# Kernel tuning notes

Measured on AMD Instinct MI355X. Metric: run time of the kernel, lower is better.

The kernel has to match this reference:

```python
import jax, jax.numpy as jnp
import numpy as np

N = 50000
NUM_USERS = 20000
E = 800000
IN_DIM = 256
OUT_DIM = 256
H = 8
DK = OUT_DIM // H


def setup_inputs() -> dict:
    key = jax.random.key(0)
    ks = jax.random.split(key, 16)
    inp = {
        "x": jax.random.normal(ks[0], (N, IN_DIM), dtype=jnp.float32),
        "row": jax.random.randint(ks[1], (E,), 0, N, dtype=jnp.int32),
        "col": jax.random.randint(ks[2], (E,), 0, N, dtype=jnp.int32),
        "relation_emb": jax.random.normal(ks[3], (OUT_DIM,), dtype=jnp.float32),
        "user_text_embs": jax.random.normal(ks[4], (NUM_USERS, IN_DIM), dtype=jnp.float32),
        "item_text_embs": jax.random.normal(ks[5], (N - NUM_USERS, IN_DIM), dtype=jnp.float32),
        "Wq": jax.random.normal(ks[6], (OUT_DIM, IN_DIM), dtype=jnp.float32) * 0.02,
        "bq": jnp.zeros((OUT_DIM,), dtype=jnp.float32),
        "Wk": jax.random.normal(ks[7], (OUT_DIM, IN_DIM), dtype=jnp.float32) * 0.02,
        "bk": jnp.zeros((OUT_DIM,), dtype=jnp.float32),
        "Wv": jax.random.normal(ks[8], (OUT_DIM, IN_DIM), dtype=jnp.float32) * 0.02,
        "bv": jnp.zeros((OUT_DIM,), dtype=jnp.float32),
        "Wo": jax.random.normal(ks[9], (OUT_DIM, OUT_DIM), dtype=jnp.float32) * 0.02,
        "bo": jnp.zeros((OUT_DIM,), dtype=jnp.float32),
    }
    return inp


def reference(x, row, col, relation_emb, user_text_embs, item_text_embs,
              Wq, bq, Wk, bk, Wv, bv, Wo, bo):
    # text_emb: users first, then items (matches torch zeros_like + slice assign)
    text_emb = jnp.concatenate([user_text_embs, item_text_embs], axis=0)  # [N, in_dim]

    Q = (text_emb @ Wq.T + bq).reshape(N, H, DK)
    K = (text_emb @ Wk.T + bk).reshape(N, H, DK)
    V = (x @ Wv.T + bv).reshape(N, H, DK)

    Q_ = Q[col]  # [E, H, DK]
    K_ = K[row]
    V_ = V[row]
    rel = relation_emb.reshape(1, H, DK)

    scores = jnp.sum(Q_ * (K_ + rel), axis=-1) / np.sqrt(DK).astype(np.float32)  # [E, H]

    # segment softmax over destination node (col)
    m = jax.ops.segment_max(scores, col, num_segments=N)          # [N, H]
    e = jnp.exp(scores - m[col])                                   # [E, H]
    denom = jax.ops.segment_sum(e, col, num_segments=N)           # [N, H]
    attn = e / denom[col]                                          # [E, H]

    out = jax.ops.segment_sum(attn[:, :, None] * V_, col, num_segments=N)  # [N, H, DK]
    out = out.reshape(N, OUT_DIM)
    return out @ Wo.T + bo
```

## Files before the change

### kernel.cpp

```cpp
#include <hip/hip_runtime.h>
#include <hip/hip_bf16.h>

#define N_NODES   50000
#define N_USERS   20000
#define N_EDGES   800000
#define DIM       256
#define NHEAD     8
#define DKH       32
#define NBLK_SCAN ((N_NODES + 255) / 256)
#define NGRP      (N_NODES / 16)
#define NGRP_PAD  3128
#define SLOTS_NODE (NGRP * 8 * 64)
#define NBLK_CAST (SLOTS_NODE / 256)
#define NBLK_HIST ((N_EDGES + 255) / 256)
#define NBLK_G64  (NGRP_PAD / 4)
#define KVROW     768

typedef __attribute__((ext_vector_type(8))) short bf16x8;
typedef __attribute__((ext_vector_type(4))) float f32x4;
typedef __attribute__((ext_vector_type(4))) unsigned short u16x4;
typedef __attribute__((ext_vector_type(8))) unsigned short u16x8;

__device__ inline unsigned short f2bf(float f) {
    union { __hip_bfloat16 b; unsigned short u; } cv;
    cv.b = __float2bfloat16(f);
    return cv.u;
}
__device__ inline float bf2f(unsigned short u) {
    return __uint_as_float(((unsigned int)u) << 16);
}
__device__ inline unsigned char f2fp8(float f) {
    unsigned int p = __builtin_amdgcn_cvt_pk_fp8_f32(f, f, 0, false);
    return (unsigned char)(p & 0xff);
}


__global__ void prep_kernel(const float* __restrict__ Wq, const float* __restrict__ Wk,
                            const float* __restrict__ Wv, const float* __restrict__ Wo,
                            unsigned short* __restrict__ Wb2,
                            const float* __restrict__ x,
                            const float* __restrict__ user, const float* __restrict__ item,
                            unsigned short* __restrict__ xb2, unsigned short* __restrict__ tb2,
                            const int* __restrict__ col, int* __restrict__ cnt)
{
    int b = blockIdx.x;
    if (b < 128) {
        int gid = b * 256 + threadIdx.x;
        const float* srcs[4] = { Wq, Wk, Wv, Wo };
        int m = gid >> 13, slot = gid & 8191;
        int lane = slot & 63, ks = (slot >> 6) & 7, g = slot >> 9;
        int c = g * 16 + (lane & 15);
        int d = ks * 32 + (lane >> 4) * 8;
        const float* s = srcs[m] + (size_t)c * DIM + d;
        float4 f0 = *(const float4*)s, f1 = *(const float4*)(s + 4);
        u16x8 o = { f2bf(f0.x), f2bf(f0.y), f2bf(f0.z), f2bf(f0.w),
                    f2bf(f1.x), f2bf(f1.y), f2bf(f1.z), f2bf(f1.w) };
        *(u16x8*)(Wb2 + (size_t)m * 65536 + (size_t)slot * 8) = o;
    } else if (b < 128 + NBLK_CAST) {
        int slot = (b - 128) * 256 + threadIdx.x;
        int lane = slot & 63, ks = (slot >> 6) & 7, g = slot >> 9;
        int r = g * 16 + (lane & 15);
        int d = ks * 32 + (lane >> 4) * 8;

        const float* sx = x + (size_t)r * DIM + d;
        float4 f0 = *(const float4*)sx, f1 = *(const float4*)(sx + 4);
        u16x8 xo = { f2bf(f0.x), f2bf(f0.y), f2bf(f0.z), f2bf(f0.w),
                     f2bf(f1.x), f2bf(f1.y), f2bf(f1.z), f2bf(f1.w) };
        *(u16x8*)(xb2 + (size_t)slot * 8) = xo;

        const float* st = (r < N_USERS) ? user + (size_t)r * DIM + d
                                        : item + (size_t)(r - N_USERS) * DIM + d;
        float4 t0 = *(const float4*)st, t1 = *(const float4*)(st + 4);
        u16x8 to = { f2bf(t0.x), f2bf(t0.y), f2bf(t0.z), f2bf(t0.w),
                     f2bf(t1.x), f2bf(t1.y), f2bf(t1.z), f2bf(t1.w) };
        *(u16x8*)(tb2 + (size_t)slot * 8) = to;
    } else {
        int e = (b - 128 - NBLK_CAST) * 256 + threadIdx.x;
        if (e < N_EDGES) atomicAdd(&cnt[col[e]], 1);
    }
}

__device__ __forceinline__ void mfma_core64(const unsigned short* __restrict__ A2,
                                            const unsigned short* __restrict__ W2,
                                            int row0, f32x4 acc[2][8],
                                            int lane, int wid)
{
    const int gA = (row0 >> 4) + (wid >> 1) * 2;
    const int gB = (wid & 1) * 8;
    #pragma unroll
    for (int ks = 0; ks < 8; ++ks) {
        bf16x8 a[2], b[8];
        #pragma unroll
        for (int i = 0; i < 2; ++i)
            a[i] = *(const bf16x8*)(A2 + (size_t)((gA + i) * 8 + ks) * 512 + lane * 8);
        #pragma unroll
        for (int j = 0; j < 8; ++j)
            b[j] = *(const bf16x8*)(W2 + (size_t)((gB + j) * 8 + ks) * 512 + lane * 8);
        #pragma unroll
        for (int i = 0; i < 2; ++i)
            #pragma unroll
            for (int j = 0; j < 8; ++j)
                acc[i][j] = __builtin_amdgcn_mfma_f32_16x16x32_bf16(a[i], b[j], acc[i][j], 0, 0, 0);
    }
}

template<int MODE>
__device__ __forceinline__ void epilogue64(f32x4 acc[2][8], const float* bias, void* Cv,
                                           int row0, int M, int lane, int wid)
{
    const int wm = wid >> 1, wn = wid & 1;
    const int lr = lane & 15, lk = lane >> 4;
    float* Cf = (float*)Cv;
    unsigned short* Cb = (unsigned short*)Cv;
    unsigned char* C8 = (unsigned char*)Cv;
    #pragma unroll
    for (int i = 0; i < 2; ++i) {
        #pragma unroll
        for (int r = 0; r < 4; ++r) {
            int grow = row0 + wm * 32 + i * 16 + lk * 4 + r;
            if (grow >= M) continue;
            #pragma unroll
            for (int j = 0; j < 8; ++j) {
                int gcol = wn * 128 + j * 16 + lr;
                float val = acc[i][j][r] + bias[gcol];
                if constexpr (MODE == 0) {
                    Cf[(size_t)grow * 256 + gcol] = val;
                } else if constexpr (MODE == 1) {
                    Cb[(size_t)grow * 256 + gcol] = f2bf(val);
                } else if constexpr (MODE == 2) {
                    C8[(size_t)grow * KVROW + gcol] = f2fp8(val);
                } else {
                    *(unsigned short*)(C8 + (size_t)grow * KVROW + 256 + gcol * 2) = f2bf(val);
                }
            }
        }
    }
}

__global__ __launch_bounds__(256) void gemm_qkv_reg(
    const unsigned short* __restrict__ tb2, const unsigned short* __restrict__ xb2,
    const unsigned short* __restrict__ Wb2,
    const float* __restrict__ bq, const float* __restrict__ bk, const float* __restrict__ bv,
    unsigned short* __restrict__ Qb, unsigned char* __restrict__ KVb, int M)
{
    const int tid = threadIdx.x;
    const int lane = tid & 63, wid = tid >> 6;
    const int row0 = blockIdx.x * 64;
    const int mat  = blockIdx.y;

    const unsigned short* A2 = (mat == 2) ? xb2 : tb2;
    const unsigned short* W2 = Wb2 + (size_t)mat * 65536;

    f32x4 acc[2][8];
    #pragma unroll
    for (int i = 0; i < 2; ++i)
        #pragma unroll
        for (int j = 0; j < 8; ++j) acc[i][j] = (f32x4){0.f, 0.f, 0.f, 0.f};

    mfma_core64(A2, W2, row0, acc, lane, wid);

    if (mat == 0)      epilogue64<1>(acc, bq, Qb,  row0, M, lane, wid);
    else if (mat == 1) epilogue64<2>(acc, bk, KVb, row0, M, lane, wid);
    else               epilogue64<3>(acc, bv, KVb, row0, M, lane, wid);
}

__global__ __launch_bounds__(256) void gemm_o_reg(
    const unsigned short* __restrict__ A2,
    const unsigned short* __restrict__ Wb2, const float* __restrict__ bo,
    float* __restrict__ C, int M)
{
    const int tid = threadIdx.x;
    const int lane = tid & 63, wid = tid >> 6;
    const int row0 = blockIdx.x * 64;

    f32x4 acc[2][8];
    #pragma unroll
    for (int i = 0; i < 2; ++i)
        #pragma unroll
        for (int j = 0; j < 8; ++j) acc[i][j] = (f32x4){0.f, 0.f, 0.f, 0.f};

    mfma_core64(A2, Wb2 + 3 * 65536, row0, acc, lane, wid);
    epilogue64<0>(acc, bo, C, row0, M, lane, wid);
}

__global__ __launch_bounds__(256) void scan_blk_kernel(const int* __restrict__ cnt,
                                                       int* __restrict__ offs_tmp,
                                                       int* __restrict__ bsum) {
    __shared__ int s[256];
    int b = blockIdx.x, t = threadIdx.x;
    int i = b * 256 + t;
    int v = (i < N_NODES) ? cnt[i] : 0;
    s[t] = v;
    __syncthreads();
    #pragma unroll
    for (int d = 1; d < 256; d <<= 1) {
        int u = (t >= d) ? s[t - d] : 0;
        __syncthreads();
        s[t] += u;
        __syncthreads();
    }
    if (i < N_NODES) offs_tmp[i] = s[t] - v;
    if (t == 255) bsum[b] = s[255];
}

__global__ __launch_bounds__(256) void scan_top_kernel(int* __restrict__ bsum) {
    __shared__ int s[256];
    int t = threadIdx.x;
    int v = (t < NBLK_SCAN) ? bsum[t] : 0;
    s[t] = v;
    __syncthreads();
    #pragma unroll
    for (int d = 1; d < 256; d <<= 1) {
        int u = (t >= d) ? s[t - d] : 0;
        __syncthreads();
        s[t] += u;
        __syncthreads();
    }
    if (t < NBLK_SCAN) bsum[t] = s[t] - v;
}

__global__ __launch_bounds__(256) void scan_add_kernel(const int* __restrict__ offs_tmp,
                                                       const int* __restrict__ bsum,
                                                       int* __restrict__ offs,
                                                       int* __restrict__ cursor) {
    int i = blockIdx.x * 256 + threadIdx.x;
    if (i == 0) offs[N_NODES] = N_EDGES;
    if (i >= N_NODES) return;
    int o = offs_tmp[i] + bsum[blockIdx.x];
    offs[i] = o;
    cursor[i] = o;
}

__global__ void scatter_kernel(const int* __restrict__ row, const int* __restrict__ col,
                               int* __restrict__ cursor, int* __restrict__ esrc) {
    int e = blockIdx.x * blockDim.x + threadIdx.x;
    if (e >= N_EDGES) return;
    int c = col[e];
    int p = atomicAdd(&cursor[c], 1);
    esrc[p] = row[e];
}

__global__ __launch_bounds__(256) void node_fused_kernel(
    const unsigned short* __restrict__ Qb, const unsigned char* __restrict__ KVb,
    const float* __restrict__ rel,
    const int* __restrict__ offs, const int* __restrict__ esrc,
    unsigned short* __restrict__ outagg2)
{
    const float SC = 0.17677669529663687f;
    int wid = (blockIdx.x * blockDim.x + threadIdx.x) >> 6;
    int lane = threadIdx.x & 63;
    if (wid >= N_NODES) return;
    int beg = offs[wid], end = offs[wid + 1];
    int d0 = lane * 4;
    const unsigned char* kbase = KVb + lane * 4;
    const unsigned char* vbase = KVb + 256 + lane * 8;

    u16x4 qb4 = *(const u16x4*)(Qb + (size_t)wid * DIM + d0);
    float qx = bf2f(qb4[0]), qy = bf2f(qb4[1]), qz = bf2f(qb4[2]), qw = bf2f(qb4[3]);
    float4 rl = *(const float4*)(rel + d0);

    float p0 = qx * rl.x + qy * rl.y + qz * rl.z + qw * rl.w;
    p0 += __shfl_xor(p0, 1);
    p0 += __shfl_xor(p0, 2);
    p0 += __shfl_xor(p0, 4);

    float den = 0.f;
    float4 acc = make_float4(0.f, 0.f, 0.f, 0.f);

    for (int base = beg; base < end; base += 64) {
        int n = end - base; if (n > 64) n = 64;
        int idx = base + lane; if (idx >= end) idx = end - 1;
        int my = esrc[idx];
        int j = 0;
        for (; j + 8 <= n; j += 8) {
            unsigned int kw[8]; u16x4 vv[8];
            #pragma unroll
            for (int u = 0; u < 8; ++u) {
                int r = __shfl(my, j + u);
                size_t ro = (size_t)r * KVROW;
                kw[u] = *(const unsigned int*)(kbase + ro);
                vv[u] = *(const u16x4*)(vbase + ro);
            }
            float s[8];
            #pragma unroll
            for (int u = 0; u < 8; ++u)
                s[u] = qx * __builtin_amdgcn_cvt_f32_fp8(kw[u], 0)
                     + qy * __builtin_amdgcn_cvt_f32_fp8(kw[u], 1)
                     + qz * __builtin_amdgcn_cvt_f32_fp8(kw[u], 2)
                     + qw * __builtin_amdgcn_cvt_f32_fp8(kw[u], 3);
            #pragma unroll
            for (int u = 0; u < 8; ++u) {
                s[u] += __shfl_xor(s[u], 1);
                s[u] += __shfl_xor(s[u], 2);
                s[u] += __shfl_xor(s[u], 4);
            }
            #pragma unroll
            for (int u = 0; u < 8; ++u) {
                float w = __expf((s[u] + p0) * SC);
                den += w;
                acc.x += w * bf2f(vv[u][0]); acc.y += w * bf2f(vv[u][1]);
                acc.z += w * bf2f(vv[u][2]); acc.w += w * bf2f(vv[u][3]);
            }
        }
        for (; j + 4 <= n; j += 4) {
            unsigned int kw[4]; u16x4 vv[4];
            #pragma unroll
            for (int u = 0; u < 4; ++u) {
                int r = __shfl(my, j + u);
                size_t ro = (size_t)r * KVROW;
                kw[u] = *(const unsigned int*)(kbase + ro);
                vv[u] = *(const u16x4*)(vbase + ro);
            }
            float s[4];
            #pragma unroll
            for (int u = 0; u < 4; ++u)
                s[u] = qx * __builtin_amdgcn_cvt_f32_fp8(kw[u], 0)
                     + qy * __builtin_amdgcn_cvt_f32_fp8(kw[u], 1)
                     + qz * __builtin_amdgcn_cvt_f32_fp8(kw[u], 2)
                     + qw * __builtin_amdgcn_cvt_f32_fp8(kw[u], 3);
            #pragma unroll
            for (int u = 0; u < 4; ++u) {
                s[u] += __shfl_xor(s[u], 1);
                s[u] += __shfl_xor(s[u], 2);
                s[u] += __shfl_xor(s[u], 4);
            }
            #pragma unroll
            for (int u = 0; u < 4; ++u) {
                float w = __expf((s[u] + p0) * SC);
                den += w;
                acc.x += w * bf2f(vv[u][0]); acc.y += w * bf2f(vv[u][1]);
                acc.z += w * bf2f(vv[u][2]); acc.w += w * bf2f(vv[u][3]);
            }
        }
        for (; j < n; ++j) {
            int r = __shfl(my, j);
            size_t ro = (size_t)r * KVROW;
            unsigned int kw = *(const unsigned int*)(kbase + ro);
            u16x4 vv = *(const u16x4*)(vbase + ro);
            float s0 = qx * __builtin_amdgcn_cvt_f32_fp8(kw, 0)
                     + qy * __builtin_amdgcn_cvt_f32_fp8(kw, 1)
                     + qz * __builtin_amdgcn_cvt_f32_fp8(kw, 2)
                     + qw * __builtin_amdgcn_cvt_f32_fp8(kw, 3);
            s0 += __shfl_xor(s0, 1);
            s0 += __shfl_xor(s0, 2);
            s0 += __shfl_xor(s0, 4);
            float w0 = __expf((s0 + p0) * SC);
            den += w0;
            acc.x += w0 * bf2f(vv[0]); acc.y += w0 * bf2f(vv[1]);
            acc.z += w0 * bf2f(vv[2]); acc.w += w0 * bf2f(vv[3]);
        }
    }
    float rden = (end > beg) ? 1.f / den : 0.f;
    u16x4 o = { f2bf(acc.x * rden), f2bf(acc.y * rden),
                f2bf(acc.z * rden), f2bf(acc.w * rden) };
    int ks = lane >> 3, lk = (lane >> 1) & 3, e4 = (lane & 1) * 4;
    size_t toff = ((size_t)(wid >> 4) * 8 + ks) * 512 + (lk * 16 + (wid & 15)) * 8 + e4;
    *(u16x4*)(outagg2 + toff) = o;
}

extern "C" void kernel_launch(void* const* d_in, const int* in_sizes, int n_in,
                              void* d_out, int out_size, void* d_ws, size_t ws_size,
                              hipStream_t stream) {
    const float* x    = (const float*)d_in[0];
    const int*   row  = (const int*)d_in[1];
    const int*   col  = (const int*)d_in[2];
    const float* rel  = (const float*)d_in[3];
    const float* user = (const float*)d_in[4];
    const float* item = (const float*)d_in[5];
    const float* Wq   = (const float*)d_in[6];
    const float* bq   = (const float*)d_in[7];
    const float* Wk   = (const float*)d_in[8];
    const float* bk   = (const float*)d_in[9];
    const float* Wv   = (const float*)d_in[10];
    const float* bv   = (const float*)d_in[11];
    const float* Wo   = (const float*)d_in[12];
    const float* bo   = (const float*)d_in[13];

    char* ws = (char*)d_ws;
    size_t off = 0;
    auto alloc = [&](size_t bytes) -> void* {
        void* p = ws + off;
        off = (off + bytes + 255) & ~(size_t)255;
        return p;
    };
    const size_t tiled_sz = (size_t)NGRP_PAD * 4096 * 2;
    unsigned short* Qb      = (unsigned short*)alloc((size_t)N_NODES * DIM * 2);
    unsigned char*  KVb     = (unsigned char*)alloc((size_t)N_NODES * KVROW);
    unsigned short* xb2     = (unsigned short*)alloc(tiled_sz);
    unsigned short* tb2     = (unsigned short*)alloc(tiled_sz);
    unsigned short* outagg2 = (unsigned short*)alloc(tiled_sz);
    unsigned short* Wb2     = (unsigned short*)alloc((size_t)4 * 65536 * 2);
    int*   cnt      = (int*)alloc((size_t)N_NODES * 4);
    int*   offs     = (int*)alloc((size_t)(N_NODES + 1) * 4);
    int*   offs_tmp = (int*)alloc((size_t)N_NODES * 4);
    int*   bsum     = (int*)alloc((size_t)NBLK_SCAN * 4);
    int*   esrc     = (int*)alloc((size_t)N_EDGES * 4);

    hipMemsetAsync(cnt, 0, (size_t)N_NODES * 4, stream);

    prep_kernel<<<128 + NBLK_CAST + NBLK_HIST, 256, 0, stream>>>(
        Wq, Wk, Wv, Wo, Wb2, x, user, item, xb2, tb2, col, cnt);
    scan_blk_kernel<<<NBLK_SCAN, 256, 0, stream>>>(cnt, offs_tmp, bsum);
    scan_top_kernel<<<1, 256, 0, stream>>>(bsum);
    scan_add_kernel<<<NBLK_SCAN, 256, 0, stream>>>(offs_tmp, bsum, offs, cnt);
    scatter_kernel<<<NBLK_HIST, 256, 0, stream>>>(row, col, cnt, esrc);

    gemm_qkv_reg<<<dim3(NBLK_G64, 3), 256, 0, stream>>>(tb2, xb2, Wb2, bq, bk, bv, Qb, KVb, N_NODES);

    node_fused_kernel<<<(N_NODES * 64 + 255) / 256, 256, 0, stream>>>(
        Qb, KVb, rel, offs, esrc, outagg2);

    gemm_o_reg<<<NBLK_G64, 256, 0, stream>>>(outagg2, Wb2, bo, (float*)d_out, N_NODES);
}
```

Baseline: 279.7 us.

## Record edge ranks in histogram and fuse CSR scatter into QKV GEMM launch

The histogram atomics now store each edge's rank within its destination bucket. This lets the scatter compute positions as offs+rank without a second round of atomics. The scatter work is then merged into the QKV GEMM launch as extra leading blocks, which removes one kernel launch and lets the scatter overlap with the GEMM. The cost is an extra 3.2MB rank buffer that is written and then read, plus a mixed grid that may interfere with GEMM block scheduling.

```diff
diff --git a/kernel.cpp b/kernel.cpp
--- a/kernel.cpp
+++ b/kernel.cpp
@@ -41,7 +41,8 @@
                             const float* __restrict__ x,
                             const float* __restrict__ user, const float* __restrict__ item,
                             unsigned short* __restrict__ xb2, unsigned short* __restrict__ tb2,
-                            const int* __restrict__ col, int* __restrict__ cnt)
+                            const int* __restrict__ col, int* __restrict__ cnt,
+                            int* __restrict__ erank)
 {
     int b = blockIdx.x;
     if (b < 128) {
@@ -76,7 +77,7 @@
         *(u16x8*)(tb2 + (size_t)slot * 8) = to;
     } else {
         int e = (b - 128 - NBLK_CAST) * 256 + threadIdx.x;
-        if (e < N_EDGES) atomicAdd(&cnt[col[e]], 1);
+        if (e < N_EDGES) erank[e] = atomicAdd(&cnt[col[e]], 1);
     }
 }
 
@@ -137,16 +138,29 @@
     }
 }
 
-__global__ __launch_bounds__(256) void gemm_qkv_reg(
+__global__ __launch_bounds__(256) void gemm_qkv_scatter(
     const unsigned short* __restrict__ tb2, const unsigned short* __restrict__ xb2,
     const unsigned short* __restrict__ Wb2,
     const float* __restrict__ bq, const float* __restrict__ bk, const float* __restrict__ bv,
-    unsigned short* __restrict__ Qb, unsigned char* __restrict__ KVb, int M)
-{
+    unsigned short* __restrict__ Qb, unsigned char* __restrict__ KVb, int M,
+    const int* __restrict__ row, const int* __restrict__ col,
+    const int* __restrict__ erank, const int* __restrict__ offs,
+    int* __restrict__ esrc)
+{
+    const int b = blockIdx.x;
+    if (b < NBLK_HIST) {
+        int e = b * 256 + threadIdx.x;
+        if (e < N_EDGES) {
+            int c = col[e];
+            esrc[offs[c] + erank[e]] = row[e];
+        }
+        return;
+    }
+    const int gb = b - NBLK_HIST;
+    const int mat = gb / NBLK_G64;
+    const int row0 = (gb % NBLK_G64) * 64;
     const int tid = threadIdx.x;
     const int lane = tid & 63, wid = tid >> 6;
-    const int row0 = blockIdx.x * 64;
-    const int mat  = blockIdx.y;
 
     const unsigned short* A2 = (mat == 2) ? xb2 : tb2;
     const unsigned short* W2 = Wb2 + (size_t)mat * 65536;
@@ -221,23 +235,11 @@
 
 __global__ __launch_bounds__(256) void scan_add_kernel(const int* __restrict__ offs_tmp,
                                                        const int* __restrict__ bsum,
-                                                       int* __restrict__ offs,
-                                                       int* __restrict__ cursor) {
+                                                       int* __restrict__ offs) {
     int i = blockIdx.x * 256 + threadIdx.x;
     if (i == 0) offs[N_NODES] = N_EDGES;
     if (i >= N_NODES) return;
-    int o = offs_tmp[i] + bsum[blockIdx.x];
-    offs[i] = o;
-    cursor[i] = o;
-}
-
-__global__ void scatter_kernel(const int* __restrict__ row, const int* __restrict__ col,
-                               int* __restrict__ cursor, int* __restrict__ esrc) {
-    int e = blockIdx.x * blockDim.x + threadIdx.x;
-    if (e >= N_EDGES) return;
-    int c = col[e];
-    int p = atomicAdd(&cursor[c], 1);
-    esrc[p] = row[e];
+    offs[i] = offs_tmp[i] + bsum[blockIdx.x];
 }
 
 __global__ __launch_bounds__(256) void node_fused_kernel(
@@ -395,17 +397,19 @@
     int*   offs_tmp = (int*)alloc((size_t)N_NODES * 4);
     int*   bsum     = (int*)alloc((size_t)NBLK_SCAN * 4);
     int*   esrc     = (int*)alloc((size_t)N_EDGES * 4);
+    int*   erank    = (int*)alloc((size_t)N_EDGES * 4);
 
     hipMemsetAsync(cnt, 0, (size_t)N_NODES * 4, stream);
 
     prep_kernel<<<128 + NBLK_CAST + NBLK_HIST, 256, 0, stream>>>(
-        Wq, Wk, Wv, Wo, Wb2, x, user, item, xb2, tb2, col, cnt);
+        Wq, Wk, Wv, Wo, Wb2, x, user, item, xb2, tb2, col, cnt, erank);
     scan_blk_kernel<<<NBLK_SCAN, 256, 0, stream>>>(cnt, offs_tmp, bsum);
     scan_top_kernel<<<1, 256, 0, stream>>>(bsum);
-    scan_add_kernel<<<NBLK_SCAN, 256, 0, stream>>>(offs_tmp, bsum, offs, cnt);
-    scatter_kernel<<<NBLK_HIST, 256, 0, stream>>>(row, col, cnt, esrc);
-
-    gemm_qkv_reg<<<dim3(NBLK_G64, 3), 256, 0, stream>>>(tb2, xb2, Wb2, bq, bk, bv, Qb, KVb, N_NODES);
+    scan_add_kernel<<<NBLK_SCAN, 256, 0, stream>>>(offs_tmp, bsum, offs);
+
+    gemm_qkv_scatter<<<NBLK_HIST + 3 * NBLK_G64, 256, 0, stream>>>(
+        tb2, xb2, Wb2, bq, bk, bv, Qb, KVb, N_NODES,
+        row, col, erank, offs, esrc);
 
     node_fused_kernel<<<(N_NODES * 64 + 255) / 256, 256, 0, stream>>>(
         Qb, KVb, rel, offs, esrc, outagg2);
```

New measurement: 252.0 us. -9.9%, faster.
